# Performance work log

Measured on AMD Instinct MI355X. Metric: run time of the kernel, lower is better.

The kernel has to match this reference:

```python
import jax, jax.numpy as jnp
import numpy as np

N, F, H, C, E = 100000, 128, 128, 40, 1600000


def setup_inputs() -> dict:
    key = jax.random.key(0)
    ks = jax.random.split(key, 8)
    x = jax.random.normal(ks[0], (N, F), dtype=jnp.float32)
    edge_index = jax.random.randint(ks[1], (2, E), 0, N, dtype=jnp.int64)
    s = 0.05
    return {
        "x": x,
        "edge_index": edge_index,
        "eps1": jnp.float32(0.0),
        "w1": jax.random.normal(ks[2], (F, H), dtype=jnp.float32) * s,
        "b1": jnp.zeros((H,), jnp.float32),
        "w2": jax.random.normal(ks[3], (H, H), dtype=jnp.float32) * s,
        "b2": jnp.zeros((H,), jnp.float32),
        "eps2": jnp.float32(0.0),
        "w3": jax.random.normal(ks[4], (H, H), dtype=jnp.float32) * s,
        "b3": jnp.zeros((H,), jnp.float32),
        "w4": jax.random.normal(ks[5], (H, C), dtype=jnp.float32) * s,
        "b4": jnp.zeros((C,), jnp.float32),
    }


def _gin_aggregate(h, src, dst, eps, n):
    # sum_{j -> i} h_j  +  (1+eps) * h_i
    agg = jax.ops.segment_sum(h[src], dst, num_segments=n)
    return (1.0 + eps) * h + agg


def reference(x, edge_index, eps1, w1, b1, w2, b2, eps2, w3, b3, w4, b4):
    src, dst = edge_index[0], edge_index[1]
    n = x.shape[0]
    # conv1: GINConv with MLP = Lin-ReLU-Lin-ReLU
    h = _gin_aggregate(x, src, dst, eps1, n)
    h = jax.nn.relu(h @ w1 + b1)
    h = jax.nn.relu(h @ w2 + b2)
    h = jax.nn.relu(h)  # outer F.relu (idempotent, kept for faithfulness)
    # dropout: identity in eval mode
    # conv2: GINConv with MLP = Lin-ReLU-Lin
    h2 = _gin_aggregate(h, src, dst, eps2, n)
    h2 = jax.nn.relu(h2 @ w3 + b3)
    h2 = h2 @ w4 + b4
    return jax.nn.log_softmax(h2, axis=1)
```

## Files before the change

### kernel.cpp

```cpp
#include <hip/hip_runtime.h>
#include <hip/hip_fp16.h>
#include <math.h>

constexpr int F = 128;
constexpr int C = 40;
constexpr int LDH = 136;
constexpr int BSHIFT = 8;
constexpr int BSIZE = 1 << BSHIFT;
constexpr int CHUNK = 4096;

typedef __attribute__((ext_vector_type(8))) _Float16 half8;
typedef __attribute__((ext_vector_type(4))) float float4v;
typedef __attribute__((ext_vector_type(2))) float floatx2;


__global__ __launch_bounds__(256) void fused_prep_kernel(
        const float* __restrict__ x, __half* __restrict__ x_h,
        unsigned char* __restrict__ xq, int n4,
        const int* __restrict__ dst, int E, int NB, int* __restrict__ coarse_count,
        const float* __restrict__ w1, const float* __restrict__ w2,
        const float* __restrict__ w3, const float* __restrict__ w4,
        __half* __restrict__ w1t, __half* __restrict__ w2t,
        __half* __restrict__ w3t, __half* __restrict__ w4t, int BA) {
    __shared__ float smem[4096];
    int b = blockIdx.x, t = threadIdx.x;
    if (b < BA) {
        int* hist = (int*)smem;
        int c0 = b * CHUNK, cend = min(c0 + CHUNK, E);
        for (int i = t; i < NB; i += 256) hist[i] = 0;
        __syncthreads();
        for (int i = c0 + t; i < cend; i += 256)
            atomicAdd(&hist[dst[i] >> BSHIFT], 1);
        __syncthreads();
        for (int i = t; i < NB; i += 256)
            if (hist[i]) atomicAdd(&coarse_count[i], hist[i]);
        return;
    }
    if (b < BA + 4) {
        const float* in; __half* outp; int Nin, Npad;
        switch (b - BA) {
            case 0:  in = w1; outp = w1t; Nin = 128; Npad = 128; break;
            case 1:  in = w2; outp = w2t; Nin = 128; Npad = 128; break;
            case 2:  in = w3; outp = w3t; Nin = 128; Npad = 128; break;
            default: in = w4; outp = w4t; Nin = 40;  Npad = 48;  break;
        }
        for (int p = 0; p < 4; ++p) {
            int nf4 = 32 * Nin / 4;
            const float4* srcv = (const float4*)(in + 32 * p * Nin);
            for (int i = t; i < nf4; i += 256) ((float4*)smem)[i] = srcv[i];
            __syncthreads();
            int total = Npad * 16;
            for (int i = t; i < total; i += 256) {
                int n = i >> 4, wl = i & 15;
                float lo = 0.f, hi = 0.f;
                if (n < Nin) {
                    lo = smem[(2 * wl) * Nin + n];
                    hi = smem[(2 * wl + 1) * Nin + n];
                }
                __half2 h = __floats2half2_rn(lo, hi);
                ((unsigned*)outp)[n * 64 + 16 * p + wl] = __builtin_bit_cast(unsigned, h);
            }
            __syncthreads();
        }
        return;
    }
    int i = (b - BA - 4) * 256 + t;
    if (i >= n4) return;
    float4 v = ((const float4*)x)[i];
    uint2 o;
    o.x = __builtin_bit_cast(unsigned, __floats2half2_rn(v.x, v.y));
    o.y = __builtin_bit_cast(unsigned, __floats2half2_rn(v.z, v.w));
    ((uint2*)x_h)[i] = o;
    unsigned p8 = __builtin_amdgcn_cvt_pk_fp8_f32(v.x, v.y, 0u, false);
    p8 = __builtin_amdgcn_cvt_pk_fp8_f32(v.z, v.w, p8, true);
    ((unsigned*)xq)[i] = p8;
}


__global__ __launch_bounds__(512) void coarse_scan_kernel(const int* __restrict__ coarse_count,
                                                          int NB, int E,
                                                          int* __restrict__ coarse_start,
                                                          int* __restrict__ bucket_pos,
                                                          int* __restrict__ row_start, int N) {
    __shared__ int tmp[512];
    int t = threadIdx.x;
    int v = (t < NB) ? coarse_count[t] : 0;
    tmp[t] = v;
    __syncthreads();
    for (int d = 1; d < 512; d <<= 1) {
        int add = (t >= d) ? tmp[t - d] : 0;
        __syncthreads();
        tmp[t] += add;
        __syncthreads();
    }
    if (t < NB) {
        int ex = tmp[t] - v;
        coarse_start[t] = ex;
        bucket_pos[t] = ex;
    }
    if (t == 0) {
        coarse_start[NB] = E;
        row_start[N] = E;
    }
}

__global__ __launch_bounds__(256) void bucket_scatter_a_kernel(
        const int* __restrict__ src, const int* __restrict__ dst, int E, int NB,
        int* __restrict__ bucket_pos, unsigned* __restrict__ pairs) {
    __shared__ int hist[512];
    __shared__ int base[512];
    int t = threadIdx.x;
    int c0 = blockIdx.x * CHUNK;
    int cend = min(c0 + CHUNK, E);
    for (int i = t; i < NB; i += 256) hist[i] = 0;
    __syncthreads();
    for (int i = c0 + t; i < cend; i += 256)
        atomicAdd(&hist[dst[i] >> BSHIFT], 1);
    __syncthreads();
    for (int i = t; i < NB; i += 256) {
        int h = hist[i];
        base[i] = (h > 0) ? atomicAdd(&bucket_pos[i], h) : 0;
        hist[i] = 0;
    }
    __syncthreads();
    for (int i = c0 + t; i < cend; i += 256) {
        int d = dst[i];
        int b = d >> BSHIFT;
        int p = base[b] + atomicAdd(&hist[b], 1);
        pairs[p] = ((unsigned)(d & (BSIZE - 1)) << 24) | (unsigned)src[i];
    }
}

__global__ __launch_bounds__(256) void bucket_sort_kernel(const unsigned* __restrict__ pairs,
                                                          const int* __restrict__ coarse_start,
                                                          int N, int* __restrict__ row_start,
                                                          int* __restrict__ src_sorted) {
    __shared__ int hist[256];
    __shared__ int tmp[256];
    int b = blockIdx.x, t = threadIdx.x;
    int base = b << BSHIFT;
    int start = coarse_start[b];
    int end = coarse_start[b + 1];
    hist[t] = 0;
    __syncthreads();
    for (int i = start + t; i < end; i += 256)
        atomicAdd(&hist[pairs[i] >> 24], 1);
    __syncthreads();
    int v = hist[t];
    tmp[t] = v;
    __syncthreads();
    for (int d = 1; d < 256; d <<= 1) {
        int add = (t >= d) ? tmp[t - d] : 0;
        __syncthreads();
        tmp[t] += add;
        __syncthreads();
    }
    int ex = start + tmp[t] - v;
    if (base + t < N) row_start[base + t] = ex;
    hist[t] = ex;
    __syncthreads();
    for (int i = start + t; i < end; i += 256) {
        unsigned u = pairs[i];
        int p = atomicAdd(&hist[u >> 24], 1);
        src_sorted[p] = (int)(u & 0x00FFFFFFu);
    }
}


__global__ __launch_bounds__(256) void agg_f16_kernel(const __half* __restrict__ feat,
        const unsigned char* __restrict__ featq,
        const int* __restrict__ row_start, const int* __restrict__ src_sorted,
        const float* __restrict__ eps_ptr, __half* __restrict__ out, int N) {
    int wid = (int)((blockIdx.x * blockDim.x + threadIdx.x) >> 6);
    int lane = threadIdx.x & 63;
    if (wid >= N) return;
    int q = lane >> 4, l16 = lane & 15;
    int s = row_start[wid], e = row_start[wid + 1];
    uint4 selfu = *(((const uint4*)(feat + (size_t)wid * F)) + l16);
    float ep1 = 1.0f + *eps_ptr;
    floatx2 accA[4], accB[4];
#pragma unroll
    for (int j = 0; j < 4; ++j) {
        accA[j] = (floatx2){0.f, 0.f};
        accB[j] = (floatx2){0.f, 0.f};
    }
    const uint2 z2 = make_uint2(0u, 0u);
    for (int i0 = s; i0 < e; i0 += 16) {
        int li = i0 + l16;
        int sv = src_sorted[li < e ? li : (e - 1)];
        int s0 = __shfl(sv, q);
        int s1 = __shfl(sv, q + 4);
        int s2 = __shfl(sv, q + 8);
        int s3 = __shfl(sv, q + 12);
        uint2 u0 = *(((const uint2*)(featq + (size_t)s0 * F)) + l16);
        uint2 u1 = *(((const uint2*)(featq + (size_t)s1 * F)) + l16);
        uint2 u2 = *(((const uint2*)(featq + (size_t)s2 * F)) + l16);
        uint2 u3 = *(((const uint2*)(featq + (size_t)s3 * F)) + l16);
        if (i0 + q >= e)      u0 = z2;
        if (i0 + q + 4 >= e)  u1 = z2;
        if (i0 + q + 8 >= e)  u2 = z2;
        if (i0 + q + 12 >= e) u3 = z2;
        accA[0] += __builtin_amdgcn_cvt_pk_f32_fp8(u0.x, false);
        accA[1] += __builtin_amdgcn_cvt_pk_f32_fp8(u0.x, true);
        accA[2] += __builtin_amdgcn_cvt_pk_f32_fp8(u0.y, false);
        accA[3] += __builtin_amdgcn_cvt_pk_f32_fp8(u0.y, true);
        accB[0] += __builtin_amdgcn_cvt_pk_f32_fp8(u1.x, false);
        accB[1] += __builtin_amdgcn_cvt_pk_f32_fp8(u1.x, true);
        accB[2] += __builtin_amdgcn_cvt_pk_f32_fp8(u1.y, false);
        accB[3] += __builtin_amdgcn_cvt_pk_f32_fp8(u1.y, true);
        accA[0] += __builtin_amdgcn_cvt_pk_f32_fp8(u2.x, false);
        accA[1] += __builtin_amdgcn_cvt_pk_f32_fp8(u2.x, true);
        accA[2] += __builtin_amdgcn_cvt_pk_f32_fp8(u2.y, false);
        accA[3] += __builtin_amdgcn_cvt_pk_f32_fp8(u2.y, true);
        accB[0] += __builtin_amdgcn_cvt_pk_f32_fp8(u3.x, false);
        accB[1] += __builtin_amdgcn_cvt_pk_f32_fp8(u3.x, true);
        accB[2] += __builtin_amdgcn_cvt_pk_f32_fp8(u3.y, false);
        accB[3] += __builtin_amdgcn_cvt_pk_f32_fp8(u3.y, true);
    }
    float a[8];
#pragma unroll
    for (int j = 0; j < 4; ++j) {
        floatx2 m = accA[j] + accB[j];
        a[2 * j] = m.x;
        a[2 * j + 1] = m.y;
    }
#pragma unroll
    for (int j = 0; j < 8; ++j) {
        a[j] += __shfl_xor(a[j], 16);
        a[j] += __shfl_xor(a[j], 32);
    }
    if (q == 0) {
        float2 s0 = __half22float2(__builtin_bit_cast(__half2, selfu.x));
        float2 s1 = __half22float2(__builtin_bit_cast(__half2, selfu.y));
        float2 s2 = __half22float2(__builtin_bit_cast(__half2, selfu.z));
        float2 s3 = __half22float2(__builtin_bit_cast(__half2, selfu.w));
        a[0] = fmaf(ep1, s0.x, a[0]); a[1] = fmaf(ep1, s0.y, a[1]);
        a[2] = fmaf(ep1, s1.x, a[2]); a[3] = fmaf(ep1, s1.y, a[3]);
        a[4] = fmaf(ep1, s2.x, a[4]); a[5] = fmaf(ep1, s2.y, a[5]);
        a[6] = fmaf(ep1, s3.x, a[6]); a[7] = fmaf(ep1, s3.y, a[7]);
        uint4 ou;
        ou.x = __builtin_bit_cast(unsigned, __floats2half2_rn(a[0], a[1]));
        ou.y = __builtin_bit_cast(unsigned, __floats2half2_rn(a[2], a[3]));
        ou.z = __builtin_bit_cast(unsigned, __floats2half2_rn(a[4], a[5]));
        ou.w = __builtin_bit_cast(unsigned, __floats2half2_rn(a[6], a[7]));
        *(((uint4*)(out + (size_t)wid * F)) + l16) = ou;
    }
}


__global__ __launch_bounds__(256) void mlp1_mfma_kernel(const __half* __restrict__ A,
        const __half* __restrict__ w1t, const float* __restrict__ b1,
        const __half* __restrict__ w2t, const float* __restrict__ b2,
        __half* __restrict__ out, unsigned char* __restrict__ outq, int N) {
    __shared__ __half ldsA[64 * LDH];
    __shared__ __half ldsW[128 * LDH];
    __shared__ float ldsB[256];
    int t = threadIdx.x;
    int wave = t >> 6, lane = t & 63, quad = lane >> 4, l16 = lane & 15;
    int br = blockIdx.x * 64;
    if (t < 128) ldsB[t] = b1[t];
    else         ldsB[t] = b2[t - 128];
    for (int i = t; i < 1024; i += 256) {
        int r = i >> 4, c = i & 15;
        int gr = br + r;
        uint4 v = make_uint4(0u, 0u, 0u, 0u);
        if (gr < N) v = *((const uint4*)(A + (size_t)gr * F + c * 8));
        *((uint4*)&ldsA[r * LDH + c * 8]) = v;
    }
    for (int i = t; i < 2048; i += 256) {
        int r = i >> 4, c = i & 15;
        *((uint4*)&ldsW[r * LDH + c * 8]) = *((const uint4*)(w1t + r * 128 + c * 8));
    }
    __syncthreads();

    int ct0 = wave * 2;
    float4v acc[4][2];
    float4v zero = {0.f, 0.f, 0.f, 0.f};
#pragma unroll
    for (int i = 0; i < 4; ++i)
#pragma unroll
        for (int j = 0; j < 2; ++j) acc[i][j] = zero;

#pragma unroll
    for (int ks = 0; ks < 4; ++ks) {
        half8 af[4], wf[2];
#pragma unroll
        for (int i = 0; i < 4; ++i)
            af[i] = *((const half8*)&ldsA[(i * 16 + l16) * LDH + ks * 32 + quad * 8]);
#pragma unroll
        for (int j = 0; j < 2; ++j)
            wf[j] = *((const half8*)&ldsW[((ct0 + j) * 16 + l16) * LDH + ks * 32 + quad * 8]);
#pragma unroll
        for (int i = 0; i < 4; ++i)
#pragma unroll
            for (int j = 0; j < 2; ++j)
                acc[i][j] = __builtin_amdgcn_mfma_f32_16x16x32_f16(wf[j], af[i], acc[i][j], 0, 0, 0);
    }
    __syncthreads();
#pragma unroll
    for (int j = 0; j < 2; ++j) {
        int c = ct0 + j;
        float4 bb = *((const float4*)&ldsB[c * 16 + quad * 4]);
#pragma unroll
        for (int i = 0; i < 4; ++i) {
            float v0 = acc[i][j][0] + bb.x; v0 = v0 > 0.f ? v0 : 0.f;
            float v1 = acc[i][j][1] + bb.y; v1 = v1 > 0.f ? v1 : 0.f;
            float v2 = acc[i][j][2] + bb.z; v2 = v2 > 0.f ? v2 : 0.f;
            float v3 = acc[i][j][3] + bb.w; v3 = v3 > 0.f ? v3 : 0.f;
            __half2 h0 = __floats2half2_rn(v0, v1);
            __half2 h1 = __floats2half2_rn(v2, v3);
            uint2 o;
            o.x = __builtin_bit_cast(unsigned, h0);
            o.y = __builtin_bit_cast(unsigned, h1);
            *((uint2*)&ldsA[(i * 16 + l16) * LDH + c * 16 + quad * 4]) = o;
        }
    }
    for (int i = t; i < 2048; i += 256) {
        int r = i >> 4, c = i & 15;
        *((uint4*)&ldsW[r * LDH + c * 8]) = *((const uint4*)(w2t + r * 128 + c * 8));
    }
    __syncthreads();

#pragma unroll
    for (int i = 0; i < 4; ++i)
#pragma unroll
        for (int j = 0; j < 2; ++j) acc[i][j] = zero;
#pragma unroll
    for (int ks = 0; ks < 4; ++ks) {
        half8 af[4], wf[2];
#pragma unroll
        for (int i = 0; i < 4; ++i)
            af[i] = *((const half8*)&ldsA[(i * 16 + l16) * LDH + ks * 32 + quad * 8]);
#pragma unroll
        for (int j = 0; j < 2; ++j)
            wf[j] = *((const half8*)&ldsW[((ct0 + j) * 16 + l16) * LDH + ks * 32 + quad * 8]);
#pragma unroll
        for (int i = 0; i < 4; ++i)
#pragma unroll
            for (int j = 0; j < 2; ++j)
                acc[i][j] = __builtin_amdgcn_mfma_f32_16x16x32_f16(wf[j], af[i], acc[i][j], 0, 0, 0);
    }
    __syncthreads();
#pragma unroll
    for (int j = 0; j < 2; ++j) {
        int c = ct0 + j;
        float4 bb = *((const float4*)&ldsB[128 + c * 16 + quad * 4]);
#pragma unroll
        for (int i = 0; i < 4; ++i) {
            float v0 = acc[i][j][0] + bb.x; v0 = v0 > 0.f ? v0 : 0.f;
            float v1 = acc[i][j][1] + bb.y; v1 = v1 > 0.f ? v1 : 0.f;
            float v2 = acc[i][j][2] + bb.z; v2 = v2 > 0.f ? v2 : 0.f;
            float v3 = acc[i][j][3] + bb.w; v3 = v3 > 0.f ? v3 : 0.f;
            __half2 h0 = __floats2half2_rn(v0, v1);
            __half2 h1 = __floats2half2_rn(v2, v3);
            uint2 o;
            o.x = __builtin_bit_cast(unsigned, h0);
            o.y = __builtin_bit_cast(unsigned, h1);
            *((uint2*)&ldsA[(i * 16 + l16) * LDH + c * 16 + quad * 4]) = o;
        }
    }
    __syncthreads();
    for (int i = t; i < 1024; i += 256) {
        int r = i >> 4, c = i & 15;
        int gr = br + r;
        if (gr < N) {
            uint4 hv = *((const uint4*)&ldsA[r * LDH + c * 8]);
            *((uint4*)(out + (size_t)gr * F + c * 8)) = hv;
            float2 f0 = __half22float2(__builtin_bit_cast(__half2, hv.x));
            float2 f1 = __half22float2(__builtin_bit_cast(__half2, hv.y));
            float2 f2 = __half22float2(__builtin_bit_cast(__half2, hv.z));
            float2 f3 = __half22float2(__builtin_bit_cast(__half2, hv.w));
            unsigned lo = __builtin_amdgcn_cvt_pk_fp8_f32(f0.x, f0.y, 0u, false);
            lo = __builtin_amdgcn_cvt_pk_fp8_f32(f1.x, f1.y, lo, true);
            unsigned hi = __builtin_amdgcn_cvt_pk_fp8_f32(f2.x, f2.y, 0u, false);
            hi = __builtin_amdgcn_cvt_pk_fp8_f32(f3.x, f3.y, hi, true);
            uint2 o8 = make_uint2(lo, hi);
            *((uint2*)(outq + (size_t)gr * F + c * 8)) = o8;
        }
    }
}


__global__ __launch_bounds__(256) void mlp2_mfma_kernel(const __half* __restrict__ A,
        const __half* __restrict__ w3t, const float* __restrict__ b3,
        const __half* __restrict__ w4t, const float* __restrict__ b4,
        float* __restrict__ out, int N) {
    __shared__ __half ldsA[64 * LDH];
    __shared__ __half ldsW[128 * LDH];
    __shared__ float ldsB[176];
    int t = threadIdx.x;
    int wave = t >> 6, lane = t & 63, quad = lane >> 4, l16 = lane & 15;
    int br = blockIdx.x * 64;
    if (t < 128) ldsB[t] = b3[t];
    else if (t < 176) ldsB[t] = (t - 128 < C) ? b4[t - 128] : 0.f;
    for (int i = t; i < 1024; i += 256) {
        int r = i >> 4, c = i & 15;
        int gr = br + r;
        uint4 v = make_uint4(0u, 0u, 0u, 0u);
        if (gr < N) v = *((const uint4*)(A + (size_t)gr * F + c * 8));
        *((uint4*)&ldsA[r * LDH + c * 8]) = v;
    }
    for (int i = t; i < 2048; i += 256) {
        int r = i >> 4, c = i & 15;
        *((uint4*)&ldsW[r * LDH + c * 8]) = *((const uint4*)(w3t + r * 128 + c * 8));
    }
    __syncthreads();

    int ct0 = wave * 2;
    float4v acc[4][2];
    float4v zero = {0.f, 0.f, 0.f, 0.f};
#pragma unroll
    for (int i = 0; i < 4; ++i)
#pragma unroll
        for (int j = 0; j < 2; ++j) acc[i][j] = zero;
#pragma unroll
    for (int ks = 0; ks < 4; ++ks) {
        half8 af[4], wf[2];
#pragma unroll
        for (int i = 0; i < 4; ++i)
            af[i] = *((const half8*)&ldsA[(i * 16 + l16) * LDH + ks * 32 + quad * 8]);
#pragma unroll
        for (int j = 0; j < 2; ++j)
            wf[j] = *((const half8*)&ldsW[((ct0 + j) * 16 + l16) * LDH + ks * 32 + quad * 8]);
#pragma unroll
        for (int i = 0; i < 4; ++i)
#pragma unroll
            for (int j = 0; j < 2; ++j)
                acc[i][j] = __builtin_amdgcn_mfma_f32_16x16x32_f16(wf[j], af[i], acc[i][j], 0, 0, 0);
    }
    __syncthreads();
#pragma unroll
    for (int j = 0; j < 2; ++j) {
        int c = ct0 + j;
        float4 bb = *((const float4*)&ldsB[c * 16 + quad * 4]);
#pragma unroll
        for (int i = 0; i < 4; ++i) {
            float v0 = acc[i][j][0] + bb.x; v0 = v0 > 0.f ? v0 : 0.f;
            float v1 = acc[i][j][1] + bb.y; v1 = v1 > 0.f ? v1 : 0.f;
            float v2 = acc[i][j][2] + bb.z; v2 = v2 > 0.f ? v2 : 0.f;
            float v3 = acc[i][j][3] + bb.w; v3 = v3 > 0.f ? v3 : 0.f;
            __half2 h0 = __floats2half2_rn(v0, v1);
            __half2 h1 = __floats2half2_rn(v2, v3);
            uint2 o;
            o.x = __builtin_bit_cast(unsigned, h0);
            o.y = __builtin_bit_cast(unsigned, h1);
            *((uint2*)&ldsA[(i * 16 + l16) * LDH + c * 16 + quad * 4]) = o;
        }
    }
    for (int i = t; i < 768; i += 256) {
        int r = i >> 4, c = i & 15;
        *((uint4*)&ldsW[r * LDH + c * 8]) = *((const uint4*)(w4t + r * 128 + c * 8));
    }
    __syncthreads();

    float4v acc4[3];
#pragma unroll
    for (int c = 0; c < 3; ++c) acc4[c] = zero;
#pragma unroll
    for (int ks = 0; ks < 4; ++ks) {
        half8 af = *((const half8*)&ldsA[(wave * 16 + l16) * LDH + ks * 32 + quad * 8]);
#pragma unroll
        for (int c = 0; c < 3; ++c) {
            half8 wf = *((const half8*)&ldsW[(c * 16 + l16) * LDH + ks * 32 + quad * 8]);
            acc4[c] = __builtin_amdgcn_mfma_f32_16x16x32_f16(wf, af, acc4[c], 0, 0, 0);
        }
    }
    float lv[3][4];
#pragma unroll
    for (int c = 0; c < 3; ++c) {
        float4 bb = *((const float4*)&ldsB[128 + c * 16 + quad * 4]);
        lv[c][0] = acc4[c][0] + bb.x;
        lv[c][1] = acc4[c][1] + bb.y;
        lv[c][2] = acc4[c][2] + bb.z;
        lv[c][3] = acc4[c][3] + bb.w;
    }
    bool tile2ok = (quad < 2);
    float m = -1e30f;
#pragma unroll
    for (int c = 0; c < 3; ++c) {
        if (c == 2 && !tile2ok) continue;
#pragma unroll
        for (int r = 0; r < 4; ++r) m = fmaxf(m, lv[c][r]);
    }
    m = fmaxf(m, __shfl_xor(m, 16));
    m = fmaxf(m, __shfl_xor(m, 32));
    float ssum = 0.f;
#pragma unroll
    for (int c = 0; c < 3; ++c) {
        if (c == 2 && !tile2ok) continue;
#pragma unroll
        for (int r = 0; r < 4; ++r) ssum += __expf(lv[c][r] - m);
    }
    ssum += __shfl_xor(ssum, 16);
    ssum += __shfl_xor(ssum, 32);
    float L = m + __logf(ssum);
    int node = br + wave * 16 + l16;
    if (node < N) {
#pragma unroll
        for (int c = 0; c < 3; ++c) {
            if (c == 2 && !tile2ok) continue;
            float4 o = make_float4(lv[c][0] - L, lv[c][1] - L, lv[c][2] - L, lv[c][3] - L);
            *((float4*)(out + (size_t)node * C + c * 16 + quad * 4)) = o;
        }
    }
}


extern "C" void kernel_launch(void* const* d_in, const int* in_sizes, int n_in,
                              void* d_out, int out_size, void* d_ws, size_t ws_size,
                              hipStream_t stream) {
    const float* x    = (const float*)d_in[0];
    const int*   ei   = (const int*)d_in[1];
    const float* eps1 = (const float*)d_in[2];
    const float* w1   = (const float*)d_in[3];
    const float* b1   = (const float*)d_in[4];
    const float* w2   = (const float*)d_in[5];
    const float* b2   = (const float*)d_in[6];
    const float* eps2 = (const float*)d_in[7];
    const float* w3   = (const float*)d_in[8];
    const float* b3   = (const float*)d_in[9];
    const float* w4   = (const float*)d_in[10];
    const float* b4   = (const float*)d_in[11];
    float* out = (float*)d_out;

    int N = in_sizes[0] / F;
    int E = in_sizes[1] / 2;
    const int* src = ei;
    const int* dst = ei + E;

    int NB = (N + BSIZE - 1) >> BSHIFT;
    int BA = (E + CHUNK - 1) / CHUNK;

    __half* x_h  = (__half*)d_ws;
    __half* h0_h = x_h + (size_t)N * F;
    __half* h_h  = h0_h + (size_t)N * F;
    __half* w1t  = h_h + (size_t)N * F;
    __half* w2t  = w1t + 128 * 128;
    __half* w3t  = w2t + 128 * 128;
    __half* w4t  = w3t + 128 * 128;
    unsigned char* fq = (unsigned char*)(w4t + 48 * 128);
    unsigned* pairs   = (unsigned*)(fq + (size_t)N * F);
    int* row_start    = (int*)(pairs + E);
    int* src_sorted   = row_start + (N + 1);
    int* coarse_count = src_sorted + E;
    int* coarse_start = coarse_count + 512;
    int* bucket_pos   = coarse_start + 513;

    int n4 = N * F / 4;
    int NCONV = (n4 + 255) / 256;

    hipMemsetAsync(coarse_count, 0, 512 * sizeof(int), stream);
    fused_prep_kernel<<<BA + 4 + NCONV, 256, 0, stream>>>(x, x_h, fq, n4, dst, E, NB,
                                                          coarse_count, w1, w2, w3, w4,
                                                          w1t, w2t, w3t, w4t, BA);

    coarse_scan_kernel<<<1, 512, 0, stream>>>(coarse_count, NB, E, coarse_start, bucket_pos,
                                              row_start, N);
    bucket_scatter_a_kernel<<<BA, 256, 0, stream>>>(src, dst, E, NB, bucket_pos, pairs);
    bucket_sort_kernel<<<NB, 256, 0, stream>>>(pairs, coarse_start, N, row_start, src_sorted);

    agg_f16_kernel<<<(N + 3) / 4, 256, 0, stream>>>(x_h, fq, row_start, src_sorted, eps1,
                                                    h0_h, N);
    mlp1_mfma_kernel<<<(N + 63) / 64, 256, 0, stream>>>(h0_h, w1t, b1, w2t, b2, h_h, fq, N);
    agg_f16_kernel<<<(N + 3) / 4, 256, 0, stream>>>(h_h, fq, row_start, src_sorted, eps2,
                                                    h0_h, N);
    mlp2_mfma_kernel<<<(N + 63) / 64, 256, 0, stream>>>(h0_h, w3t, b3, w4t, b4, out, N);
}
```

Baseline: 307.7 us.

## Fold coarse scan into scatter/sort kernels and prescale gather offsets with dummy row

```diff
diff --git a/kernel.cpp b/kernel.cpp
--- a/kernel.cpp
+++ b/kernel.cpp
@@ -21,7 +21,7 @@
         const float* __restrict__ w1, const float* __restrict__ w2,
         const float* __restrict__ w3, const float* __restrict__ w4,
         __half* __restrict__ w1t, __half* __restrict__ w2t,
-        __half* __restrict__ w3t, __half* __restrict__ w4t, int BA) {
+        __half* __restrict__ w3t, __half* __restrict__ w4t, int BA, int N) {
     __shared__ float smem[4096];
     int b = blockIdx.x, t = threadIdx.x;
     if (b < BA) {
@@ -62,6 +62,8 @@
             }
             __syncthreads();
         }
+        if (b - BA == 3 && t < 8)
+            *(((uint4*)(xq + (size_t)N * F)) + t) = make_uint4(0u, 0u, 0u, 0u);
         return;
     }
     int i = (b - BA - 4) * 256 + t;
@@ -77,53 +79,35 @@
 }
 
 
-__global__ __launch_bounds__(512) void coarse_scan_kernel(const int* __restrict__ coarse_count,
-                                                          int NB, int E,
-                                                          int* __restrict__ coarse_start,
-                                                          int* __restrict__ bucket_pos,
-                                                          int* __restrict__ row_start, int N) {
-    __shared__ int tmp[512];
-    int t = threadIdx.x;
-    int v = (t < NB) ? coarse_count[t] : 0;
-    tmp[t] = v;
-    __syncthreads();
-    for (int d = 1; d < 512; d <<= 1) {
-        int add = (t >= d) ? tmp[t - d] : 0;
-        __syncthreads();
-        tmp[t] += add;
-        __syncthreads();
-    }
-    if (t < NB) {
-        int ex = tmp[t] - v;
-        coarse_start[t] = ex;
-        bucket_pos[t] = ex;
-    }
-    if (t == 0) {
-        coarse_start[NB] = E;
-        row_start[N] = E;
-    }
-}
-
-__global__ __launch_bounds__(256) void bucket_scatter_a_kernel(
+__global__ __launch_bounds__(512) void bucket_scatter_kernel(
         const int* __restrict__ src, const int* __restrict__ dst, int E, int NB,
-        int* __restrict__ bucket_pos, unsigned* __restrict__ pairs) {
+        const int* __restrict__ coarse_count, int* __restrict__ pos0,
+        unsigned* __restrict__ pairs) {
+    __shared__ int scn[512];
     __shared__ int hist[512];
     __shared__ int base[512];
     int t = threadIdx.x;
-    int c0 = blockIdx.x * CHUNK;
-    int cend = min(c0 + CHUNK, E);
-    for (int i = t; i < NB; i += 256) hist[i] = 0;
-    __syncthreads();
-    for (int i = c0 + t; i < cend; i += 256)
+    int v = (t < NB) ? coarse_count[t] : 0;
+    scn[t] = v;
+    __syncthreads();
+    for (int d = 1; d < 512; d <<= 1) {
+        int add = (t >= d) ? scn[t - d] : 0;
+        __syncthreads();
+        scn[t] += add;
+        __syncthreads();
+    }
+    int cstart = scn[t] - v;
+    hist[t] = 0;
+    __syncthreads();
+    int c0 = blockIdx.x * CHUNK, cend = min(c0 + CHUNK, E);
+    for (int i = c0 + t; i < cend; i += 512)
         atomicAdd(&hist[dst[i] >> BSHIFT], 1);
     __syncthreads();
-    for (int i = t; i < NB; i += 256) {
-        int h = hist[i];
-        base[i] = (h > 0) ? atomicAdd(&bucket_pos[i], h) : 0;
-        hist[i] = 0;
-    }
-    __syncthreads();
-    for (int i = c0 + t; i < cend; i += 256) {
+    int h = hist[t];
+    base[t] = (h > 0) ? (cstart + atomicAdd(&pos0[t], h)) : 0;
+    hist[t] = 0;
+    __syncthreads();
+    for (int i = c0 + t; i < cend; i += 512) {
         int d = dst[i];
         int b = d >> BSHIFT;
         int p = base[b] + atomicAdd(&hist[b], 1);
@@ -131,45 +115,60 @@
     }
 }
 
-__global__ __launch_bounds__(256) void bucket_sort_kernel(const unsigned* __restrict__ pairs,
-                                                          const int* __restrict__ coarse_start,
-                                                          int N, int* __restrict__ row_start,
-                                                          int* __restrict__ src_sorted) {
+__global__ __launch_bounds__(512) void bucket_sort_kernel(const unsigned* __restrict__ pairs,
+                                                          const int* __restrict__ coarse_count,
+                                                          int NB, int N, int E,
+                                                          int* __restrict__ row_start,
+                                                          unsigned* __restrict__ src_sorted) {
+    __shared__ int scn[512];
     __shared__ int hist[256];
     __shared__ int tmp[256];
     int b = blockIdx.x, t = threadIdx.x;
+    int v = (t < NB) ? coarse_count[t] : 0;
+    scn[t] = v;
+    __syncthreads();
+    for (int d = 1; d < 512; d <<= 1) {
+        int add = (t >= d) ? scn[t - d] : 0;
+        __syncthreads();
+        scn[t] += add;
+        __syncthreads();
+    }
+    int end = scn[b];
+    int start = end - coarse_count[b];
     int base = b << BSHIFT;
-    int start = coarse_start[b];
-    int end = coarse_start[b + 1];
-    hist[t] = 0;
-    __syncthreads();
-    for (int i = start + t; i < end; i += 256)
+    if (t < 256) hist[t] = 0;
+    __syncthreads();
+    for (int i = start + t; i < end; i += 512)
         atomicAdd(&hist[pairs[i] >> 24], 1);
     __syncthreads();
-    int v = hist[t];
-    tmp[t] = v;
+    int hv = (t < 256) ? hist[t] : 0;
+    if (t < 256) tmp[t] = hv;
     __syncthreads();
     for (int d = 1; d < 256; d <<= 1) {
-        int add = (t >= d) ? tmp[t - d] : 0;
-        __syncthreads();
-        tmp[t] += add;
-        __syncthreads();
-    }
-    int ex = start + tmp[t] - v;
-    if (base + t < N) row_start[base + t] = ex;
-    hist[t] = ex;
-    __syncthreads();
-    for (int i = start + t; i < end; i += 256) {
+        int add = (t >= d && t < 256) ? tmp[t - d] : 0;
+        __syncthreads();
+        if (t < 256) tmp[t] += add;
+        __syncthreads();
+    }
+    if (t < 256) {
+        int ex = start + tmp[t] - hv;
+        if (base + t < N) row_start[base + t] = ex;
+        hist[t] = ex;
+    }
+    __syncthreads();
+    for (int i = start + t; i < end; i += 512) {
         unsigned u = pairs[i];
         int p = atomicAdd(&hist[u >> 24], 1);
-        src_sorted[p] = (int)(u & 0x00FFFFFFu);
-    }
+        src_sorted[p] = (u & 0x00FFFFFFu) << 7;
+    }
+    if (b == NB - 1 && t < 32) src_sorted[E + t] = ((unsigned)N) << 7;
+    if (b == 0 && t == 0) row_start[N] = E;
 }
 
 
 __global__ __launch_bounds__(256) void agg_f16_kernel(const __half* __restrict__ feat,
         const unsigned char* __restrict__ featq,
-        const int* __restrict__ row_start, const int* __restrict__ src_sorted,
+        const int* __restrict__ row_start, const unsigned* __restrict__ src_sorted,
         const float* __restrict__ eps_ptr, __half* __restrict__ out, int N) {
     int wid = (int)((blockIdx.x * blockDim.x + threadIdx.x) >> 6);
     int lane = threadIdx.x & 63;
@@ -178,28 +177,28 @@
     int s = row_start[wid], e = row_start[wid + 1];
     uint4 selfu = *(((const uint4*)(feat + (size_t)wid * F)) + l16);
     float ep1 = 1.0f + *eps_ptr;
+    const unsigned dummy = ((unsigned)N) << 7;
+    const unsigned char* fb = featq + l16 * 8;
     floatx2 accA[4], accB[4];
 #pragma unroll
     for (int j = 0; j < 4; ++j) {
         accA[j] = (floatx2){0.f, 0.f};
         accB[j] = (floatx2){0.f, 0.f};
     }
-    const uint2 z2 = make_uint2(0u, 0u);
     for (int i0 = s; i0 < e; i0 += 16) {
-        int li = i0 + l16;
-        int sv = src_sorted[li < e ? li : (e - 1)];
-        int s0 = __shfl(sv, q);
-        int s1 = __shfl(sv, q + 4);
-        int s2 = __shfl(sv, q + 8);
-        int s3 = __shfl(sv, q + 12);
-        uint2 u0 = *(((const uint2*)(featq + (size_t)s0 * F)) + l16);
-        uint2 u1 = *(((const uint2*)(featq + (size_t)s1 * F)) + l16);
-        uint2 u2 = *(((const uint2*)(featq + (size_t)s2 * F)) + l16);
-        uint2 u3 = *(((const uint2*)(featq + (size_t)s3 * F)) + l16);
-        if (i0 + q >= e)      u0 = z2;
-        if (i0 + q + 4 >= e)  u1 = z2;
-        if (i0 + q + 8 >= e)  u2 = z2;
-        if (i0 + q + 12 >= e) u3 = z2;
+        unsigned off = src_sorted[i0 + l16];
+        unsigned o0 = (unsigned)__shfl((int)off, q);
+        unsigned o1 = (unsigned)__shfl((int)off, q + 4);
+        unsigned o2 = (unsigned)__shfl((int)off, q + 8);
+        unsigned o3 = (unsigned)__shfl((int)off, q + 12);
+        o0 = (i0 + q < e) ? o0 : dummy;
+        o1 = (i0 + q + 4 < e) ? o1 : dummy;
+        o2 = (i0 + q + 8 < e) ? o2 : dummy;
+        o3 = (i0 + q + 12 < e) ? o3 : dummy;
+        uint2 u0 = *((const uint2*)(fb + o0));
+        uint2 u1 = *((const uint2*)(fb + o1));
+        uint2 u2 = *((const uint2*)(fb + o2));
+        uint2 u3 = *((const uint2*)(fb + o3));
         accA[0] += __builtin_amdgcn_cvt_pk_f32_fp8(u0.x, false);
         accA[1] += __builtin_amdgcn_cvt_pk_f32_fp8(u0.x, true);
         accA[2] += __builtin_amdgcn_cvt_pk_f32_fp8(u0.y, false);
@@ -539,25 +538,23 @@
     __half* w3t  = w2t + 128 * 128;
     __half* w4t  = w3t + 128 * 128;
     unsigned char* fq = (unsigned char*)(w4t + 48 * 128);
-    unsigned* pairs   = (unsigned*)(fq + (size_t)N * F);
+    unsigned* pairs   = (unsigned*)(fq + (size_t)(N + 1) * F);
     int* row_start    = (int*)(pairs + E);
-    int* src_sorted   = row_start + (N + 1);
-    int* coarse_count = src_sorted + E;
-    int* coarse_start = coarse_count + 512;
-    int* bucket_pos   = coarse_start + 513;
+    unsigned* src_sorted = (unsigned*)(row_start + (N + 1));
+    int* coarse_count = (int*)(src_sorted + E + 32);
+    int* pos0         = coarse_count + 512;
 
     int n4 = N * F / 4;
     int NCONV = (n4 + 255) / 256;
 
-    hipMemsetAsync(coarse_count, 0, 512 * sizeof(int), stream);
+    hipMemsetAsync(coarse_count, 0, 1024 * sizeof(int), stream);
     fused_prep_kernel<<<BA + 4 + NCONV, 256, 0, stream>>>(x, x_h, fq, n4, dst, E, NB,
                                                           coarse_count, w1, w2, w3, w4,
-                                                          w1t, w2t, w3t, w4t, BA);
-
-    coarse_scan_kernel<<<1, 512, 0, stream>>>(coarse_count, NB, E, coarse_start, bucket_pos,
-                                              row_start, N);
-    bucket_scatter_a_kernel<<<BA, 256, 0, stream>>>(src, dst, E, NB, bucket_pos, pairs);
-    bucket_sort_kernel<<<NB, 256, 0, stream>>>(pairs, coarse_start, N, row_start, src_sorted);
+                                                          w1t, w2t, w3t, w4t, BA, N);
+
+    bucket_scatter_kernel<<<BA, 512, 0, stream>>>(src, dst, E, NB, coarse_count, pos0, pairs);
+    bucket_sort_kernel<<<NB, 512, 0, stream>>>(pairs, coarse_count, NB, N, E, row_start,
+                                               src_sorted);
 
     agg_f16_kernel<<<(N + 3) / 4, 256, 0, stream>>>(x_h, fq, row_start, src_sorted, eps1,
                                                     h0_h, N);
```

Result: faster. 293.5 us (-4.6%).
